# Optimization experiments

Measured on AMD Instinct MI355X. Metric: run time of the kernel, lower is better.

Reference implementation:

```python
import jax, jax.numpy as jnp
import numpy as np

MARGIN = 5.0


def setup_inputs() -> dict:
    key = jax.random.key(0)
    k1, k2, k3 = jax.random.split(key, 3)
    N, D = 8192, 4096
    recon_x = jax.random.normal(k1, (N, D), dtype=jnp.float32)
    x = jax.random.normal(k2, (N, D), dtype=jnp.float32)
    targets = jax.random.randint(k3, (N,), 0, 2, dtype=jnp.int64)
    return {"recon_x": recon_x, "x": x, "targets": targets}


def reference(recon_x, x, targets):
    # per-sample L2 distance between recon_x and x: [N]
    d = jnp.sqrt(jnp.sum((recon_x - x) ** 2, axis=1)) + 0.001
    pos = targets == 1  # anchor-positive samples -> dist_ap
    neg = targets == 0  # negative samples       -> dist_an
    # all pos-neg pairs: MarginRankingLoss(dist_an, dist_ap, y=1)
    #   = mean over pairs of max(0, dist_ap - dist_an + margin)
    pair_mask = pos[:, None] & neg[None, :]  # [N, N]
    elem = jnp.maximum(d[:, None] - d[None, :] + MARGIN, 0.0)
    cnt = jnp.sum(pair_mask).astype(elem.dtype)
    return jnp.sum(jnp.where(pair_mask, elem, 0.0)) / cnt
```

## Files before the change

kernel.cpp:

```cpp
#include <hip/hip_runtime.h>
#include <math.h>

#define N_ROWS 8192
#define D_COLS 4096
#define MARGIN 5.0f
#define PAIR_BLOCKS 1024

__global__ __launch_bounds__(256) void dist_kernel(
    const float* __restrict__ rx, const float* __restrict__ x,
    const int* __restrict__ tgt, float* __restrict__ dp, float* __restrict__ dn,
    double* __restrict__ sum, int* __restrict__ ticket, int* __restrict__ npos) {
  if (blockIdx.x == 0 && threadIdx.x == 0) { *sum = 0.0; *ticket = 0; *npos = 0; }
  const int lane = threadIdx.x & 63;
  const int row  = blockIdx.x * 4 + (threadIdx.x >> 6);
  const float4* a = reinterpret_cast<const float4*>(rx) + (size_t)row * (D_COLS / 4);
  const float4* b = reinterpret_cast<const float4*>(x)  + (size_t)row * (D_COLS / 4);
  float s = 0.f;
#pragma unroll
  for (int k = 0; k < D_COLS / 4 / 64; ++k) {
    float4 va = a[lane + k * 64];
    float4 vb = b[lane + k * 64];
    float d0 = va.x - vb.x, d1 = va.y - vb.y, d2 = va.z - vb.z, d3 = va.w - vb.w;
    s = fmaf(d0, d0, s); s = fmaf(d1, d1, s);
    s = fmaf(d2, d2, s); s = fmaf(d3, d3, s);
  }
#pragma unroll
  for (int off = 32; off; off >>= 1) s += __shfl_down(s, off, 64);
  if (lane == 0) {
    float dd = sqrtf(s) + 0.001f;
    int t = tgt[row];
    dp[row] = (t == 1) ? dd : -INFINITY;
    dn[row] = (t == 0) ? dd : INFINITY;
  }
}

__global__ __launch_bounds__(256) void pair_kernel(
    const float* __restrict__ dp, const float* __restrict__ dn,
    double* __restrict__ sum, int* __restrict__ ticket, int* __restrict__ npos,
    float* __restrict__ out) {
  float r[N_ROWS / 256];
#pragma unroll
  for (int k = 0; k < N_ROWS / 256; ++k) r[k] = dn[threadIdx.x + k * 256];
  float acc = 0.f;
  int cnt = 0;
  for (int i = blockIdx.x; i < N_ROWS; i += PAIR_BLOCKS) {
    float dpi = dp[i];
    if (dpi == -INFINITY) continue;
    ++cnt;
    float dpi5 = dpi + MARGIN;
#pragma unroll
    for (int k = 0; k < N_ROWS / 256; ++k) acc += fmaxf(dpi5 - r[k], 0.f);
  }
#pragma unroll
  for (int off = 32; off; off >>= 1) acc += __shfl_down(acc, off, 64);
  __shared__ float ws[4];
  const int lane = threadIdx.x & 63, wid = threadIdx.x >> 6;
  if (lane == 0) ws[wid] = acc;
  __syncthreads();
  if (threadIdx.x == 0) {
    atomicAdd(sum, (double)(ws[0] + ws[1] + ws[2] + ws[3]));
    atomicAdd(npos, cnt);
    __threadfence();
    int t = atomicAdd(ticket, 1);
    if (t == PAIR_BLOCKS - 1) {
      double s = atomicAdd(sum, 0.0);
      long long np = (long long)atomicAdd(npos, 0);
      long long c = np * (long long)(N_ROWS - np);
      out[0] = (float)(s / (double)c);
    }
  }
}

extern "C" void kernel_launch(void* const* d_in, const int* in_sizes, int n_in,
                              void* d_out, int out_size, void* d_ws, size_t ws_size,
                              hipStream_t stream) {
  const float* rx  = (const float*)d_in[0];
  const float* x   = (const float*)d_in[1];
  const int*   tgt = (const int*)d_in[2];
  float* out = (float*)d_out;

  float*  dp     = (float*)d_ws;
  float*  dn     = dp + N_ROWS;
  double* sum    = (double*)(dn + N_ROWS);
  int*    ticket = (int*)(sum + 1);
  int*    npos   = ticket + 1;

  dist_kernel<<<N_ROWS / 4, 256, 0, stream>>>(rx, x, tgt, dp, dn, sum, ticket, npos);
  pair_kernel<<<PAIR_BLOCKS, 256, 0, stream>>>(dp, dn, sum, ticket, npos, out);
}
```

Before: 315.3 us.

## Batch distance loads and replace atomic ticket reduction with a final kernel

The distance kernel now loads 8 float4s from each input before computing, and uses two accumulators to raise memory-level parallelism. The pair kernel drops to 256 blocks and writes per-block partial sums. A third single-block kernel reduces the partials in double precision and counts positives. This removes the global atomics and ticket logic at the cost of one extra kernel launch. Per-block partials are now accumulated in float rather than sent to a double atomic.

```diff
diff --git a/kernel.cpp b/kernel.cpp
--- a/kernel.cpp
+++ b/kernel.cpp
@@ -4,26 +4,32 @@
 #define N_ROWS 8192
 #define D_COLS 4096
 #define MARGIN 5.0f
-#define PAIR_BLOCKS 1024
+#define PAIR_BLOCKS 256
 
 __global__ __launch_bounds__(256) void dist_kernel(
     const float* __restrict__ rx, const float* __restrict__ x,
-    const int* __restrict__ tgt, float* __restrict__ dp, float* __restrict__ dn,
-    double* __restrict__ sum, int* __restrict__ ticket, int* __restrict__ npos) {
-  if (blockIdx.x == 0 && threadIdx.x == 0) { *sum = 0.0; *ticket = 0; *npos = 0; }
+    const int* __restrict__ tgt, float* __restrict__ dp, float* __restrict__ dn) {
   const int lane = threadIdx.x & 63;
   const int row  = blockIdx.x * 4 + (threadIdx.x >> 6);
   const float4* a = reinterpret_cast<const float4*>(rx) + (size_t)row * (D_COLS / 4);
   const float4* b = reinterpret_cast<const float4*>(x)  + (size_t)row * (D_COLS / 4);
-  float s = 0.f;
+  float s0 = 0.f, s1 = 0.f;
+#pragma unroll 1
+  for (int c = 0; c < D_COLS / 4 / 64 / 8; ++c) {
+    float4 va[8], vb[8];
 #pragma unroll
-  for (int k = 0; k < D_COLS / 4 / 64; ++k) {
-    float4 va = a[lane + k * 64];
-    float4 vb = b[lane + k * 64];
-    float d0 = va.x - vb.x, d1 = va.y - vb.y, d2 = va.z - vb.z, d3 = va.w - vb.w;
-    s = fmaf(d0, d0, s); s = fmaf(d1, d1, s);
-    s = fmaf(d2, d2, s); s = fmaf(d3, d3, s);
+    for (int u = 0; u < 8; ++u) va[u] = a[lane + (c * 8 + u) * 64];
+#pragma unroll
+    for (int u = 0; u < 8; ++u) vb[u] = b[lane + (c * 8 + u) * 64];
+#pragma unroll
+    for (int u = 0; u < 8; ++u) {
+      float d0 = va[u].x - vb[u].x, d1 = va[u].y - vb[u].y;
+      float d2 = va[u].z - vb[u].z, d3 = va[u].w - vb[u].w;
+      s0 = fmaf(d0, d0, s0); s1 = fmaf(d1, d1, s1);
+      s0 = fmaf(d2, d2, s0); s1 = fmaf(d3, d3, s1);
+    }
   }
+  float s = s0 + s1;
 #pragma unroll
   for (int off = 32; off; off >>= 1) s += __shfl_down(s, off, 64);
   if (lane == 0) {
@@ -36,17 +42,15 @@
 
 __global__ __launch_bounds__(256) void pair_kernel(
     const float* __restrict__ dp, const float* __restrict__ dn,
-    double* __restrict__ sum, int* __restrict__ ticket, int* __restrict__ npos,
-    float* __restrict__ out) {
+    float* __restrict__ partial) {
   float r[N_ROWS / 256];
 #pragma unroll
   for (int k = 0; k < N_ROWS / 256; ++k) r[k] = dn[threadIdx.x + k * 256];
   float acc = 0.f;
-  int cnt = 0;
+#pragma unroll 1
   for (int i = blockIdx.x; i < N_ROWS; i += PAIR_BLOCKS) {
     float dpi = dp[i];
     if (dpi == -INFINITY) continue;
-    ++cnt;
     float dpi5 = dpi + MARGIN;
 #pragma unroll
     for (int k = 0; k < N_ROWS / 256; ++k) acc += fmaxf(dpi5 - r[k], 0.f);
@@ -57,17 +61,32 @@
   const int lane = threadIdx.x & 63, wid = threadIdx.x >> 6;
   if (lane == 0) ws[wid] = acc;
   __syncthreads();
+  if (threadIdx.x == 0) partial[blockIdx.x] = ws[0] + ws[1] + ws[2] + ws[3];
+}
+
+__global__ __launch_bounds__(256) void final_kernel(
+    const float* __restrict__ dp, const float* __restrict__ partial,
+    float* __restrict__ out) {
+  double s = (double)partial[threadIdx.x];
+  int c = 0;
+#pragma unroll
+  for (int k = 0; k < N_ROWS / 256; ++k)
+    c += (dp[threadIdx.x + k * 256] != -INFINITY);
+#pragma unroll
+  for (int off = 32; off; off >>= 1) {
+    s += __shfl_down(s, off, 64);
+    c += __shfl_down(c, off, 64);
+  }
+  __shared__ double sws[4];
+  __shared__ int cws[4];
+  const int lane = threadIdx.x & 63, wid = threadIdx.x >> 6;
+  if (lane == 0) { sws[wid] = s; cws[wid] = c; }
+  __syncthreads();
   if (threadIdx.x == 0) {
-    atomicAdd(sum, (double)(ws[0] + ws[1] + ws[2] + ws[3]));
-    atomicAdd(npos, cnt);
-    __threadfence();
-    int t = atomicAdd(ticket, 1);
-    if (t == PAIR_BLOCKS - 1) {
-      double s = atomicAdd(sum, 0.0);
-      long long np = (long long)atomicAdd(npos, 0);
-      long long c = np * (long long)(N_ROWS - np);
-      out[0] = (float)(s / (double)c);
-    }
+    double tot = sws[0] + sws[1] + sws[2] + sws[3];
+    long long np = cws[0] + cws[1] + cws[2] + cws[3];
+    long long cnt = np * (long long)(N_ROWS - np);
+    out[0] = (float)(tot / (double)cnt);
   }
 }
 
@@ -79,12 +98,11 @@
   const int*   tgt = (const int*)d_in[2];
   float* out = (float*)d_out;
 
-  float*  dp     = (float*)d_ws;
-  float*  dn     = dp + N_ROWS;
-  double* sum    = (double*)(dn + N_ROWS);
-  int*    ticket = (int*)(sum + 1);
-  int*    npos   = ticket + 1;
+  float* dp      = (float*)d_ws;
+  float* dn      = dp + N_ROWS;
+  float* partial = dn + N_ROWS;
 
-  dist_kernel<<<N_ROWS / 4, 256, 0, stream>>>(rx, x, tgt, dp, dn, sum, ticket, npos);
-  pair_kernel<<<PAIR_BLOCKS, 256, 0, stream>>>(dp, dn, sum, ticket, npos, out);
+  dist_kernel<<<N_ROWS / 4, 256, 0, stream>>>(rx, x, tgt, dp, dn);
+  pair_kernel<<<PAIR_BLOCKS, 256, 0, stream>>>(dp, dn, partial);
+  final_kernel<<<1, 256, 0, stream>>>(dp, partial, out);
 }
```

After: 290.8 us. 1.08x faster.
